# Optimization experiments

Measured on AMD Instinct MI355X. Metric: run time of the kernel, lower is better.

Reference implementation:

```python
import jax, jax.numpy as jnp
import numpy as np

D_MODEL = 1024
NUM_HEADS = 16
HEAD_DIM = D_MODEL // NUM_HEADS
B, S = 2, 2048
EPS = 1e-8


def setup_inputs() -> dict:
    key = jax.random.key(0)
    ks = jax.random.split(key, 9)
    sc = 1.0 / np.sqrt(D_MODEL)
    return {
        "x": jax.random.normal(ks[0], (B, S, D_MODEL), jnp.float32),
        "wq": jax.random.normal(ks[1], (D_MODEL, D_MODEL), jnp.float32) * sc,
        "bq": jax.random.normal(ks[2], (D_MODEL,), jnp.float32) * 0.01,
        "wk": jax.random.normal(ks[3], (D_MODEL, D_MODEL), jnp.float32) * sc,
        "bk": jax.random.normal(ks[4], (D_MODEL,), jnp.float32) * 0.01,
        "wv": jax.random.normal(ks[5], (D_MODEL, D_MODEL), jnp.float32) * sc,
        "bv": jax.random.normal(ks[6], (D_MODEL,), jnp.float32) * 0.01,
        "wo": jax.random.normal(ks[7], (D_MODEL, D_MODEL), jnp.float32) * sc,
        "bo": jax.random.normal(ks[8], (D_MODEL,), jnp.float32) * 0.01,
    }


def reference(x, wq, bq, wk, bk, wv, bv, wo, bo):
    b, s, d = x.shape
    h, hd = NUM_HEADS, HEAD_DIM
    # projections (torch Linear: y = x W^T + b); reshape to [b, h, s, hd]
    def proj(w, bias):
        return (jnp.einsum('bsd,ed->bse', x, w) + bias).reshape(b, s, h, hd).transpose(0, 2, 1, 3)
    q = proj(wq, bq)
    k = proj(wk, bk)
    v = proj(wv, bv)
    scores = jnp.einsum('bhqd,bhkd->bhqk', q, k) / np.sqrt(hd)
    attn = jax.nn.softmax(scores, axis=-1)
    o = jnp.einsum('bhqk,bhkd->bhqd', attn, v)  # [b, h, s, hd]
    # per-position, per-head Gram-Schmidt exclusion: remove component of o[i]
    # along v[i] (the loop in the original is independent over positions)
    v_norm_sq = jnp.sum(v * v, axis=-1, keepdims=True)          # [b,h,s,1]
    align = jnp.sum(o * v, axis=-1, keepdims=True) / (v_norm_sq + EPS)
    o = o - align * v
    o = o.transpose(0, 2, 1, 3).reshape(b, s, d)
    return jnp.einsum('bsd,ed->bse', o, wo) + bo
```

## Files before the change

### kernel.cpp

```cpp
#include <hip/hip_runtime.h>
#include <stdint.h>

#define SEQ 2048
#define NTOK 4096
#define DM 1024

typedef __bf16 bf16x8 __attribute__((ext_vector_type(8)));
typedef __bf16 bf16x4 __attribute__((ext_vector_type(4)));
typedef float f32x4 __attribute__((ext_vector_type(4)));

__device__ __forceinline__ unsigned short f2bf(float f) {
  union { float f; unsigned u; } v; v.f = f;
  return (unsigned short)((v.u + 0x7fffu + ((v.u >> 16) & 1u)) >> 16);
}
__device__ __forceinline__ float bf2f(unsigned short s) {
  union { unsigned u; float f; } v; v.u = ((unsigned)s) << 16; return v.f;
}
__device__ __forceinline__ unsigned pkbf(float a, float b) {
  union { float f; unsigned u; } x, y; x.f = a; y.f = b;
  return __builtin_amdgcn_perm(y.u + 0x8000u, x.u + 0x8000u, 0x07060302u);
}

__device__ __forceinline__ void async16(const unsigned short* g, unsigned short* l) {
  __builtin_amdgcn_global_load_lds(
      (const __attribute__((address_space(1))) void*)g,
      (__attribute__((address_space(3))) void*)l, 16, 0, 0);
}

__global__ __launch_bounds__(256) void cast_all(
    const float* __restrict__ x, const float* __restrict__ wq,
    const float* __restrict__ wk, const float* __restrict__ wv,
    const float* __restrict__ wo, unsigned short* __restrict__ dst) {
  size_t i = ((size_t)blockIdx.x * 256 + threadIdx.x) * 4;
  const float* src; size_t off;
  if (i < (size_t)NTOK * DM) { src = x; off = i; }
  else {
    size_t j = i - (size_t)NTOK * DM;
    int s = (int)(j >> 20);
    src = (s == 0) ? wq : (s == 1) ? wk : (s == 2) ? wv : wo;
    off = j & 1048575u;
  }
  float4 f = *(const float4*)(src + off);
  ushort4 o;
  o.x = f2bf(f.x); o.y = f2bf(f.y); o.z = f2bf(f.z); o.w = f2bf(f.w);
  *(ushort4*)(dst + i) = o;
}

__device__ __forceinline__ void gemm128_core(
    const unsigned short* __restrict__ A, const unsigned short* __restrict__ Bw,
    int m0, int n0, f32x4 acc[4][4], unsigned short* As, unsigned short* Bs) {
  const int tid = threadIdx.x;
  const int lane = tid & 63;
  const int w = tid >> 6;
  const int wm = (w >> 1) * 64, wn = (w & 1) * 64;
  const int quad = lane >> 4, l16 = lane & 15;
  const int srow = tid >> 2, scol = (tid & 3) * 8;

  for (int kt = 0; kt < 1024; kt += 32) {
    __syncthreads();
    async16(A + (size_t)(m0 + srow) * 1024 + kt + scol, As + srow * 32 + scol);
    async16(A + (size_t)(m0 + 64 + srow) * 1024 + kt + scol, As + (64 + srow) * 32 + scol);
    async16(Bw + (size_t)(n0 + srow) * 1024 + kt + scol, Bs + srow * 32 + scol);
    async16(Bw + (size_t)(n0 + 64 + srow) * 1024 + kt + scol, Bs + (64 + srow) * 32 + scol);
    __syncthreads();
    bf16x8 af[4], bf[4];
#pragma unroll
    for (int i = 0; i < 4; ++i)
      af[i] = *(const bf16x8*)(As + (wm + i * 16 + l16) * 32 + quad * 8);
#pragma unroll
    for (int j = 0; j < 4; ++j)
      bf[j] = *(const bf16x8*)(Bs + (wn + j * 16 + l16) * 32 + quad * 8);
#pragma unroll
    for (int i = 0; i < 4; ++i)
#pragma unroll
      for (int j = 0; j < 4; ++j)
        acc[i][j] = __builtin_amdgcn_mfma_f32_16x16x32_bf16(af[i], bf[j], acc[i][j], 0, 0, 0);
  }
}

__global__ __launch_bounds__(256) void qkv_gemm(
    const unsigned short* __restrict__ xb,
    const unsigned short* __restrict__ wqb, const unsigned short* __restrict__ wkb,
    const unsigned short* __restrict__ wvb,
    const float* __restrict__ bq, const float* __restrict__ bk, const float* __restrict__ bv,
    unsigned short* __restrict__ Q, unsigned short* __restrict__ Kd,
    unsigned short* __restrict__ Vt) {
  __shared__ unsigned short As[128 * 32], Bs[128 * 32];
  const int kind = blockIdx.z;
  const unsigned short* A; const unsigned short* Bw;
  int m0, n0;
  if (kind == 2) { A = wvb; Bw = xb; m0 = blockIdx.x * 128; n0 = blockIdx.y * 128; }
  else { A = xb; Bw = (kind == 0) ? wqb : wkb; m0 = blockIdx.y * 128; n0 = blockIdx.x * 128; }
  f32x4 acc[4][4];
#pragma unroll
  for (int i = 0; i < 4; ++i)
#pragma unroll
    for (int j = 0; j < 4; ++j) { f32x4 z = {0.f, 0.f, 0.f, 0.f}; acc[i][j] = z; }
  gemm128_core(A, Bw, m0, n0, acc, As, Bs);

  const int lane = threadIdx.x & 63, w = threadIdx.x >> 6;
  const int quad = lane >> 4, l16 = lane & 15;
  const int wm = (w >> 1) * 64, wn = (w & 1) * 64;

  if (kind == 2) {
#pragma unroll
    for (int i = 0; i < 4; ++i)
#pragma unroll
      for (int j = 0; j < 4; ++j) {
        const int n = n0 + wn + j * 16 + l16;
        const int tb = n >> 11, s = n & 2047;
#pragma unroll
        for (int r = 0; r < 4; ++r) {
          const int m = m0 + wm + i * 16 + quad * 4 + r;
          const int h = m >> 6, d = m & 63;
          Vt[((size_t)(tb * 16 + h) * 64 + d) * SEQ + s] = f2bf(acc[i][j][r] + bv[m]);
        }
      }
  } else {
    const float* bias = (kind == 0) ? bq : bk;
    const float scale = (kind == 0) ? 0.180336880f : 1.0f;
#pragma unroll
    for (int i = 0; i < 4; ++i)
#pragma unroll
      for (int j = 0; j < 4; ++j) {
        const int col = n0 + wn + j * 16 + l16;
        const float bb = bias[col];
        const int h = col >> 6, d = col & 63;
#pragma unroll
        for (int r = 0; r < 4; ++r) {
          const int m = m0 + wm + i * 16 + quad * 4 + r;
          const int b = m >> 11, s = m & 2047;
          const int bh = b * 16 + h;
          const unsigned short val = f2bf((acc[i][j][r] + bb) * scale);
          if (kind == 0) Q[((size_t)bh * SEQ + s) * 64 + d] = val;
          else           Kd[((size_t)bh * SEQ + s) * 64 + d] = val;
        }
      }
  }
}

__global__ __launch_bounds__(256) void attn_kernel(
    const unsigned short* __restrict__ Q, const unsigned short* __restrict__ Kd,
    const unsigned short* __restrict__ Vt,
    unsigned short* __restrict__ Op, float* __restrict__ Lp) {
  __shared__ unsigned short KV[4][4096];
  const int gx = blockIdx.x;
  const int xcd = gx & 7;
  const int idx = gx >> 3;
  const int bh  = xcd * 4 + (idx & 3);
  const int ksl = (idx >> 2) & 1;
  const int q0  = ((idx >> 3) & 15) * 128;
  const int ks0 = ksl << 10;
  const int tid = threadIdx.x, lane = tid & 63, w = tid >> 6;
  const int quad = lane >> 4, l16 = lane & 15;
  const unsigned short* Qp = Q + (size_t)bh * SEQ * 64;
  const unsigned short* Kp = Kd + (size_t)bh * SEQ * 64;
  const unsigned short* Vp = Vt + (size_t)bh * 64 * SEQ;
  const int srow = tid >> 3;
  const int sc = ((tid & 7) ^ (srow & 7)) << 3;

#pragma unroll
  for (int c = 0; c < 4; ++c)
    async16(Qp + (size_t)(q0 + c * 32 + srow) * 64 + sc,
            KV[(c < 2) ? 1 : 3] + (c & 1) * 2048 + tid * 8);
  async16(Kp + (size_t)(ks0 + srow) * 64 + sc, KV[0] + tid * 8);
  async16(Kp + (size_t)(ks0 + 32 + srow) * 64 + sc, KV[0] + 2048 + tid * 8);
  async16(Vp + (size_t)srow * SEQ + ks0 + sc, KV[2] + tid * 8);
  async16(Vp + (size_t)(32 + srow) * SEQ + ks0 + sc, KV[2] + 2048 + tid * 8);
  __syncthreads();

  const int sel = l16 & 7;
  const unsigned short* Qsrc = (w < 2) ? KV[1] : KV[3];
  bf16x8 bQ[2][2];
#pragma unroll
  for (int qq = 0; qq < 2; ++qq) {
    const int qrow = (w * 32 + qq * 16 + l16) & 63;
#pragma unroll
    for (int hh = 0; hh < 2; ++hh)
      bQ[qq][hh] = *(const bf16x8*)(Qsrc + qrow * 64 + (((hh * 4 + quad) ^ sel) << 3));
  }
  __syncthreads();

  union { unsigned short u[8]; bf16x8 v; } one8;
#pragma unroll
  for (int t = 0; t < 8; ++t) one8.u[t] = 0x3F80;
  const bf16x8 aOnes = one8.v;

  f32x4 o_acc[2][4];
  f32x4 l_acc[2];
  const f32x4 zinit = {-12.f, -12.f, -12.f, -12.f};
#pragma unroll
  for (int qq = 0; qq < 2; ++qq) {
    f32x4 z = {0.f, 0.f, 0.f, 0.f};
    l_acc[qq] = z;
#pragma unroll
    for (int dt = 0; dt < 4; ++dt) o_acc[qq][dt] = z;
  }

  for (int it = 0; it < 16; ++it) {
    const int cur = it & 1;
    if (it) __syncthreads();
    if (it + 1 < 16) {
      const int kt = ks0 + (it + 1) * 64, nb = (it + 1) & 1;
      async16(Kp + (size_t)(kt + srow) * 64 + sc, KV[nb] + tid * 8);
      async16(Kp + (size_t)(kt + 32 + srow) * 64 + sc, KV[nb] + 2048 + tid * 8);
      async16(Vp + (size_t)srow * SEQ + kt + sc, KV[2 + nb] + tid * 8);
      async16(Vp + (size_t)(32 + srow) * SEQ + kt + sc, KV[2 + nb] + 2048 + tid * 8);
    }
    const unsigned short* Ks = KV[cur];
    const unsigned short* Vs = KV[2 + cur];

    f32x4 st[2][4];
#pragma unroll
    for (int kk = 0; kk < 4; ++kk) {
      const int krow = kk * 16 + l16;
      bf16x8 a0 = *(const bf16x8*)(Ks + krow * 64 + ((quad ^ sel) << 3));
      bf16x8 a1 = *(const bf16x8*)(Ks + krow * 64 + (((4 + quad) ^ sel) << 3));
#pragma unroll
      for (int qq = 0; qq < 2; ++qq) {
        f32x4 z = __builtin_amdgcn_mfma_f32_16x16x32_bf16(a0, bQ[qq][0], zinit, 0, 0, 0);
        z = __builtin_amdgcn_mfma_f32_16x16x32_bf16(a1, bQ[qq][1], z, 0, 0, 0);
        st[qq][kk] = z;
      }
    }

    bf16x8 bP[2][2];
#pragma unroll
    for (int qq = 0; qq < 2; ++qq) {
#pragma unroll
      for (int kk = 0; kk < 4; ++kk)
#pragma unroll
        for (int r = 0; r < 4; ++r)
          st[qq][kk][r] = __builtin_amdgcn_exp2f(st[qq][kk][r]);
#pragma unroll
      for (int G = 0; G < 2; ++G) {
        union { unsigned d[4]; bf16x8 v; } pk;
        pk.d[0] = pkbf(st[qq][2 * G][0], st[qq][2 * G][1]);
        pk.d[1] = pkbf(st[qq][2 * G][2], st[qq][2 * G][3]);
        pk.d[2] = pkbf(st[qq][2 * G + 1][0], st[qq][2 * G + 1][1]);
        pk.d[3] = pkbf(st[qq][2 * G + 1][2], st[qq][2 * G + 1][3]);
        bP[qq][G] = pk.v;
      }
    }

#pragma unroll
    for (int qq = 0; qq < 2; ++qq)
#pragma unroll
      for (int G = 0; G < 2; ++G)
        l_acc[qq] = __builtin_amdgcn_mfma_f32_16x16x32_bf16(aOnes, bP[qq][G], l_acc[qq], 0, 0, 0);

#pragma unroll
    for (int dt = 0; dt < 4; ++dt) {
      const unsigned short* vbase = Vs + (dt * 16 + l16) * 64;
      const int inner = (quad & 1) * 4;
#pragma unroll
      for (int G = 0; G < 2; ++G) {
        const int c0 = 4 * G + (quad >> 1);
        bf16x4 lo = *(const bf16x4*)(vbase + ((c0 ^ sel) << 3) + inner);
        bf16x4 hi = *(const bf16x4*)(vbase + (((c0 + 2) ^ sel) << 3) + inner);
        bf16x8 aV = __builtin_shufflevector(lo, hi, 0, 1, 2, 3, 4, 5, 6, 7);
#pragma unroll
        for (int qq = 0; qq < 2; ++qq)
          o_acc[qq][dt] = __builtin_amdgcn_mfma_f32_16x16x32_bf16(aV, bP[qq][G], o_acc[qq][dt], 0, 0, 0);
      }
    }
  }

  const size_t sb = (size_t)(ksl * 32 + bh);
#pragma unroll
  for (int qq = 0; qq < 2; ++qq) {
    const int qg = q0 + w * 32 + qq * 16 + l16;
#pragma unroll
    for (int dt = 0; dt < 4; ++dt)
#pragma unroll
      for (int r = 0; r < 4; ++r) {
        const int d = dt * 16 + quad * 4 + r;
        Op[(sb * 64 + d) * SEQ + qg] = f2bf(o_acc[qq][dt][r]);
      }
    if (quad == 0) Lp[sb * SEQ + qg] = l_acc[qq][0];
  }
}

__global__ __launch_bounds__(128) void combine_kernel(
    const unsigned short* __restrict__ Op, const float* __restrict__ Lp,
    const unsigned short* __restrict__ Vt, unsigned short* __restrict__ O) {
  const int bh = blockIdx.y;
  const int q = blockIdx.x * 128 + threadIdx.x;
  const size_t QC = (size_t)32 * SEQ;
  const size_t idx = (size_t)bh * SEQ + q;
  const float inv = 1.0f / (Lp[idx] + Lp[QC + idx]);
  const unsigned short* O1 = Op + (size_t)bh * 64 * SEQ + q;
  const unsigned short* O2 = O1 + QC * 64;
  const unsigned short* Vp = Vt + (size_t)bh * 64 * SEQ + q;
  float o64[64];
  float ov = 0.f, vv = 0.f;
#pragma unroll
  for (int d = 0; d < 64; ++d) {
    const float o = (bf2f(O1[(size_t)d * SEQ]) + bf2f(O2[(size_t)d * SEQ])) * inv;
    const float v = bf2f(Vp[(size_t)d * SEQ]);
    o64[d] = o; ov += o * v; vv += v * v;
  }
  const float align = ov / (vv + 1e-8f);
  const int b = bh >> 4, h = bh & 15;
  unsigned short* dst = O + (size_t)(b * SEQ + q) * DM + h * 64;
#pragma unroll
  for (int d = 0; d < 64; d += 2) {
    const float a0 = o64[d]     - align * bf2f(Vp[(size_t)d * SEQ]);
    const float a1 = o64[d + 1] - align * bf2f(Vp[(size_t)(d + 1) * SEQ]);
    *(unsigned*)(dst + d) = pkbf(a0, a1);
  }
}

__global__ __launch_bounds__(256) void out_gemm(
    const unsigned short* __restrict__ Ob, const unsigned short* __restrict__ wob,
    const float* __restrict__ bo, float* __restrict__ out) {
  __shared__ unsigned short As[64 * 32], Bs[128 * 32];
  const int m0 = blockIdx.y * 64, n0 = blockIdx.x * 128;
  const int tid = threadIdx.x, lane = tid & 63, w = tid >> 6;
  const int wm = (w >> 1) * 32, wn = (w & 1) * 64;
  const int quad = lane >> 4, l16 = lane & 15;
  const int srow = tid >> 2, scol = (tid & 3) * 8;
  f32x4 acc[2][4];
#pragma unroll
  for (int i = 0; i < 2; ++i)
#pragma unroll
    for (int j = 0; j < 4; ++j) { f32x4 z = {0.f, 0.f, 0.f, 0.f}; acc[i][j] = z; }

  for (int kt = 0; kt < 1024; kt += 32) {
    __syncthreads();
    async16(Ob + (size_t)(m0 + srow) * 1024 + kt + scol, As + srow * 32 + scol);
    async16(wob + (size_t)(n0 + srow) * 1024 + kt + scol, Bs + srow * 32 + scol);
    async16(wob + (size_t)(n0 + 64 + srow) * 1024 + kt + scol, Bs + (64 + srow) * 32 + scol);
    __syncthreads();
    bf16x8 af[2], bf[4];
#pragma unroll
    for (int i = 0; i < 2; ++i)
      af[i] = *(const bf16x8*)(As + (wm + i * 16 + l16) * 32 + quad * 8);
#pragma unroll
    for (int j = 0; j < 4; ++j)
      bf[j] = *(const bf16x8*)(Bs + (wn + j * 16 + l16) * 32 + quad * 8);
#pragma unroll
    for (int i = 0; i < 2; ++i)
#pragma unroll
      for (int j = 0; j < 4; ++j)
        acc[i][j] = __builtin_amdgcn_mfma_f32_16x16x32_bf16(af[i], bf[j], acc[i][j], 0, 0, 0);
  }

#pragma unroll
  for (int i = 0; i < 2; ++i)
#pragma unroll
    for (int j = 0; j < 4; ++j) {
      const int col = n0 + wn + j * 16 + l16;
      const float bb = bo[col];
#pragma unroll
      for (int r = 0; r < 4; ++r) {
        const int m = m0 + wm + i * 16 + quad * 4 + r;
        out[(size_t)m * DM + col] = acc[i][j][r] + bb;
      }
    }
}

extern "C" void kernel_launch(void* const* d_in, const int* in_sizes, int n_in,
                              void* d_out, int out_size, void* d_ws, size_t ws_size,
                              hipStream_t stream) {
  const float* x  = (const float*)d_in[0];
  const float* wq = (const float*)d_in[1];
  const float* bq = (const float*)d_in[2];
  const float* wk = (const float*)d_in[3];
  const float* bk = (const float*)d_in[4];
  const float* wv = (const float*)d_in[5];
  const float* bv = (const float*)d_in[6];
  const float* wo = (const float*)d_in[7];
  const float* bo = (const float*)d_in[8];
  float* out = (float*)d_out;
  (void)in_sizes; (void)n_in; (void)out_size; (void)ws_size;

  unsigned short* ws  = (unsigned short*)d_ws;
  unsigned short* xb  = ws;
  unsigned short* wqb = xb + (size_t)NTOK * DM;
  unsigned short* wkb = wqb + (size_t)DM * DM;
  unsigned short* wvb = wkb + (size_t)DM * DM;
  unsigned short* wob = wvb + (size_t)DM * DM;
  unsigned short* Qb  = wob + (size_t)DM * DM;
  unsigned short* Kb  = Qb + (size_t)NTOK * DM;
  unsigned short* Vtb = Kb + (size_t)NTOK * DM;
  unsigned short* Ob  = Vtb + (size_t)NTOK * DM;
  unsigned short* Opb = Ob + (size_t)NTOK * DM;
  float* Lpw = (float*)(Opb + (size_t)2 * 32 * 64 * SEQ);

  cast_all<<<8192, 256, 0, stream>>>(x, wq, wk, wv, wo, ws);
  qkv_gemm<<<dim3(8, 32, 3), 256, 0, stream>>>(xb, wqb, wkb, wvb, bq, bk, bv, Qb, Kb, Vtb);
  attn_kernel<<<1024, 256, 0, stream>>>(Qb, Kb, Vtb, Opb, Lpw);
  combine_kernel<<<dim3(16, 32), 128, 0, stream>>>(Opb, Lpw, Vtb, Ob);
  out_gemm<<<dim3(8, 64), 256, 0, stream>>>(Ob, wob, bo, out);
}
```

Before: 211.2 us.

## Double GEMM K-tile to 64 with swizzled LDS and widen attention query tile

The QKV and output GEMMs now stage 64-wide K slices, using an XOR-swizzled LDS layout. This halves the number of barrier-separated iterations and is meant to avoid bank conflicts on fragment reads. The attention kernel now gives each block 256 queries, with 64 per wave, launches half as many blocks, and fuses the exp/pack step into the score loop. This amortizes K/V tile loads over more queries, at the cost of more registers (launch bounds 256,2) and fewer blocks for load balancing.

```diff
diff --git a/kernel.cpp b/kernel.cpp
--- a/kernel.cpp
+++ b/kernel.cpp
@@ -46,35 +46,39 @@
   *(ushort4*)(dst + i) = o;
 }
 
-__device__ __forceinline__ void gemm128_core(
+__device__ __forceinline__ void gemm128_bk64(
     const unsigned short* __restrict__ A, const unsigned short* __restrict__ Bw,
     int m0, int n0, f32x4 acc[4][4], unsigned short* As, unsigned short* Bs) {
-  const int tid = threadIdx.x;
-  const int lane = tid & 63;
-  const int w = tid >> 6;
+  const int tid = threadIdx.x, lane = tid & 63, w = tid >> 6;
   const int wm = (w >> 1) * 64, wn = (w & 1) * 64;
-  const int quad = lane >> 4, l16 = lane & 15;
-  const int srow = tid >> 2, scol = (tid & 3) * 8;
-
-  for (int kt = 0; kt < 1024; kt += 32) {
+  const int quad = lane >> 4, l16 = lane & 15, sel = l16 & 7;
+  const int srow = tid >> 3;
+  const int sc = ((tid & 7) ^ (srow & 7)) << 3;
+
+  for (int kt = 0; kt < 1024; kt += 64) {
     __syncthreads();
-    async16(A + (size_t)(m0 + srow) * 1024 + kt + scol, As + srow * 32 + scol);
-    async16(A + (size_t)(m0 + 64 + srow) * 1024 + kt + scol, As + (64 + srow) * 32 + scol);
-    async16(Bw + (size_t)(n0 + srow) * 1024 + kt + scol, Bs + srow * 32 + scol);
-    async16(Bw + (size_t)(n0 + 64 + srow) * 1024 + kt + scol, Bs + (64 + srow) * 32 + scol);
+#pragma unroll
+    for (int c = 0; c < 4; ++c) {
+      const int row = c * 32 + srow;
+      async16(A + (size_t)(m0 + row) * 1024 + kt + sc, As + c * 2048 + tid * 8);
+      async16(Bw + (size_t)(n0 + row) * 1024 + kt + sc, Bs + c * 2048 + tid * 8);
+    }
     __syncthreads();
-    bf16x8 af[4], bf[4];
-#pragma unroll
-    for (int i = 0; i < 4; ++i)
-      af[i] = *(const bf16x8*)(As + (wm + i * 16 + l16) * 32 + quad * 8);
-#pragma unroll
-    for (int j = 0; j < 4; ++j)
-      bf[j] = *(const bf16x8*)(Bs + (wn + j * 16 + l16) * 32 + quad * 8);
-#pragma unroll
-    for (int i = 0; i < 4; ++i)
+#pragma unroll
+    for (int ks = 0; ks < 2; ++ks) {
+      bf16x8 af[4], bf[4];
+#pragma unroll
+      for (int i = 0; i < 4; ++i)
+        af[i] = *(const bf16x8*)(As + (wm + i * 16 + l16) * 64 + (((ks * 4 + quad) ^ sel) << 3));
 #pragma unroll
       for (int j = 0; j < 4; ++j)
-        acc[i][j] = __builtin_amdgcn_mfma_f32_16x16x32_bf16(af[i], bf[j], acc[i][j], 0, 0, 0);
+        bf[j] = *(const bf16x8*)(Bs + (wn + j * 16 + l16) * 64 + (((ks * 4 + quad) ^ sel) << 3));
+#pragma unroll
+      for (int i = 0; i < 4; ++i)
+#pragma unroll
+        for (int j = 0; j < 4; ++j)
+          acc[i][j] = __builtin_amdgcn_mfma_f32_16x16x32_bf16(af[i], bf[j], acc[i][j], 0, 0, 0);
+    }
   }
 }
 
@@ -85,7 +89,7 @@
     const float* __restrict__ bq, const float* __restrict__ bk, const float* __restrict__ bv,
     unsigned short* __restrict__ Q, unsigned short* __restrict__ Kd,
     unsigned short* __restrict__ Vt) {
-  __shared__ unsigned short As[128 * 32], Bs[128 * 32];
+  __shared__ unsigned short As[128 * 64], Bs[128 * 64];
   const int kind = blockIdx.z;
   const unsigned short* A; const unsigned short* Bw;
   int m0, n0;
@@ -96,7 +100,7 @@
   for (int i = 0; i < 4; ++i)
 #pragma unroll
     for (int j = 0; j < 4; ++j) { f32x4 z = {0.f, 0.f, 0.f, 0.f}; acc[i][j] = z; }
-  gemm128_core(A, Bw, m0, n0, acc, As, Bs);
+  gemm128_bk64(A, Bw, m0, n0, acc, As, Bs);
 
   const int lane = threadIdx.x & 63, w = threadIdx.x >> 6;
   const int quad = lane >> 4, l16 = lane & 15;
@@ -139,7 +143,7 @@
   }
 }
 
-__global__ __launch_bounds__(256) void attn_kernel(
+__global__ __launch_bounds__(256, 2) void attn_kernel(
     const unsigned short* __restrict__ Q, const unsigned short* __restrict__ Kd,
     const unsigned short* __restrict__ Vt,
     unsigned short* __restrict__ Op, float* __restrict__ Lp) {
@@ -149,7 +153,7 @@
   const int idx = gx >> 3;
   const int bh  = xcd * 4 + (idx & 3);
   const int ksl = (idx >> 2) & 1;
-  const int q0  = ((idx >> 3) & 15) * 128;
+  const int q0  = (idx >> 3) * 256;
   const int ks0 = ksl << 10;
   const int tid = threadIdx.x, lane = tid & 63, w = tid >> 6;
   const int quad = lane >> 4, l16 = lane & 15;
@@ -160,37 +164,38 @@
   const int sc = ((tid & 7) ^ (srow & 7)) << 3;
 
 #pragma unroll
-  for (int c = 0; c < 4; ++c)
+  for (int c = 0; c < 8; ++c)
     async16(Qp + (size_t)(q0 + c * 32 + srow) * 64 + sc,
-            KV[(c < 2) ? 1 : 3] + (c & 1) * 2048 + tid * 8);
+            KV[c >> 1] + (c & 1) * 2048 + tid * 8);
+  __syncthreads();
+
+  const int sel = l16 & 7;
+  const unsigned short* Qsrc = KV[w];
+  bf16x8 bQ[4][2];
+#pragma unroll
+  for (int qq = 0; qq < 4; ++qq) {
+    const int qrow = qq * 16 + l16;
+#pragma unroll
+    for (int hh = 0; hh < 2; ++hh)
+      bQ[qq][hh] = *(const bf16x8*)(Qsrc + qrow * 64 + (((hh * 4 + quad) ^ sel) << 3));
+  }
+  __syncthreads();
+
   async16(Kp + (size_t)(ks0 + srow) * 64 + sc, KV[0] + tid * 8);
   async16(Kp + (size_t)(ks0 + 32 + srow) * 64 + sc, KV[0] + 2048 + tid * 8);
   async16(Vp + (size_t)srow * SEQ + ks0 + sc, KV[2] + tid * 8);
   async16(Vp + (size_t)(32 + srow) * SEQ + ks0 + sc, KV[2] + 2048 + tid * 8);
-  __syncthreads();
-
-  const int sel = l16 & 7;
-  const unsigned short* Qsrc = (w < 2) ? KV[1] : KV[3];
-  bf16x8 bQ[2][2];
-#pragma unroll
-  for (int qq = 0; qq < 2; ++qq) {
-    const int qrow = (w * 32 + qq * 16 + l16) & 63;
-#pragma unroll
-    for (int hh = 0; hh < 2; ++hh)
-      bQ[qq][hh] = *(const bf16x8*)(Qsrc + qrow * 64 + (((hh * 4 + quad) ^ sel) << 3));
-  }
-  __syncthreads();
 
   union { unsigned short u[8]; bf16x8 v; } one8;
 #pragma unroll
   for (int t = 0; t < 8; ++t) one8.u[t] = 0x3F80;
   const bf16x8 aOnes = one8.v;
 
-  f32x4 o_acc[2][4];
-  f32x4 l_acc[2];
+  f32x4 o_acc[4][4];
+  f32x4 l_acc[4];
   const f32x4 zinit = {-12.f, -12.f, -12.f, -12.f};
 #pragma unroll
-  for (int qq = 0; qq < 2; ++qq) {
+  for (int qq = 0; qq < 4; ++qq) {
     f32x4 z = {0.f, 0.f, 0.f, 0.f};
     l_acc[qq] = z;
 #pragma unroll
@@ -199,7 +204,7 @@
 
   for (int it = 0; it < 16; ++it) {
     const int cur = it & 1;
-    if (it) __syncthreads();
+    __syncthreads();
     if (it + 1 < 16) {
       const int kt = ks0 + (it + 1) * 64, nb = (it + 1) & 1;
       async16(Kp + (size_t)(kt + srow) * 64 + sc, KV[nb] + tid * 8);
@@ -210,41 +215,30 @@
     const unsigned short* Ks = KV[cur];
     const unsigned short* Vs = KV[2 + cur];
 
-    f32x4 st[2][4];
+    bf16x8 bP[4][2];
 #pragma unroll
     for (int kk = 0; kk < 4; ++kk) {
       const int krow = kk * 16 + l16;
       bf16x8 a0 = *(const bf16x8*)(Ks + krow * 64 + ((quad ^ sel) << 3));
       bf16x8 a1 = *(const bf16x8*)(Ks + krow * 64 + (((4 + quad) ^ sel) << 3));
 #pragma unroll
-      for (int qq = 0; qq < 2; ++qq) {
+      for (int qq = 0; qq < 4; ++qq) {
         f32x4 z = __builtin_amdgcn_mfma_f32_16x16x32_bf16(a0, bQ[qq][0], zinit, 0, 0, 0);
         z = __builtin_amdgcn_mfma_f32_16x16x32_bf16(a1, bQ[qq][1], z, 0, 0, 0);
-        st[qq][kk] = z;
-      }
-    }
-
-    bf16x8 bP[2][2];
-#pragma unroll
-    for (int qq = 0; qq < 2; ++qq) {
-#pragma unroll
-      for (int kk = 0; kk < 4; ++kk)
-#pragma unroll
-        for (int r = 0; r < 4; ++r)
-          st[qq][kk][r] = __builtin_amdgcn_exp2f(st[qq][kk][r]);
-#pragma unroll
-      for (int G = 0; G < 2; ++G) {
+#pragma unroll
+        for (int r = 0; r < 4; ++r) z[r] = __builtin_amdgcn_exp2f(z[r]);
+        unsigned lo = pkbf(z[0], z[1]);
+        unsigned hi = pkbf(z[2], z[3]);
         union { unsigned d[4]; bf16x8 v; } pk;
-        pk.d[0] = pkbf(st[qq][2 * G][0], st[qq][2 * G][1]);
-        pk.d[1] = pkbf(st[qq][2 * G][2], st[qq][2 * G][3]);
-        pk.d[2] = pkbf(st[qq][2 * G + 1][0], st[qq][2 * G + 1][1]);
-        pk.d[3] = pkbf(st[qq][2 * G + 1][2], st[qq][2 * G + 1][3]);
-        bP[qq][G] = pk.v;
-      }
-    }
-
-#pragma unroll
-    for (int qq = 0; qq < 2; ++qq)
+        pk.v = bP[qq][kk >> 1];
+        pk.d[(kk & 1) * 2] = lo;
+        pk.d[(kk & 1) * 2 + 1] = hi;
+        bP[qq][kk >> 1] = pk.v;
+      }
+    }
+
+#pragma unroll
+    for (int qq = 0; qq < 4; ++qq)
 #pragma unroll
       for (int G = 0; G < 2; ++G)
         l_acc[qq] = __builtin_amdgcn_mfma_f32_16x16x32_bf16(aOnes, bP[qq][G], l_acc[qq], 0, 0, 0);
@@ -260,7 +254,7 @@
         bf16x4 hi = *(const bf16x4*)(vbase + (((c0 + 2) ^ sel) << 3) + inner);
         bf16x8 aV = __builtin_shufflevector(lo, hi, 0, 1, 2, 3, 4, 5, 6, 7);
 #pragma unroll
-        for (int qq = 0; qq < 2; ++qq)
+        for (int qq = 0; qq < 4; ++qq)
           o_acc[qq][dt] = __builtin_amdgcn_mfma_f32_16x16x32_bf16(aV, bP[qq][G], o_acc[qq][dt], 0, 0, 0);
       }
     }
@@ -268,8 +262,8 @@
 
   const size_t sb = (size_t)(ksl * 32 + bh);
 #pragma unroll
-  for (int qq = 0; qq < 2; ++qq) {
-    const int qg = q0 + w * 32 + qq * 16 + l16;
+  for (int qq = 0; qq < 4; ++qq) {
+    const int qg = q0 + w * 64 + qq * 16 + l16;
 #pragma unroll
     for (int dt = 0; dt < 4; ++dt)
 #pragma unroll
@@ -314,36 +308,47 @@
 __global__ __launch_bounds__(256) void out_gemm(
     const unsigned short* __restrict__ Ob, const unsigned short* __restrict__ wob,
     const float* __restrict__ bo, float* __restrict__ out) {
-  __shared__ unsigned short As[64 * 32], Bs[128 * 32];
+  __shared__ unsigned short As[64 * 64], Bs[128 * 64];
   const int m0 = blockIdx.y * 64, n0 = blockIdx.x * 128;
   const int tid = threadIdx.x, lane = tid & 63, w = tid >> 6;
   const int wm = (w >> 1) * 32, wn = (w & 1) * 64;
-  const int quad = lane >> 4, l16 = lane & 15;
-  const int srow = tid >> 2, scol = (tid & 3) * 8;
+  const int quad = lane >> 4, l16 = lane & 15, sel = l16 & 7;
+  const int srow = tid >> 3;
+  const int sc = ((tid & 7) ^ (srow & 7)) << 3;
   f32x4 acc[2][4];
 #pragma unroll
   for (int i = 0; i < 2; ++i)
 #pragma unroll
     for (int j = 0; j < 4; ++j) { f32x4 z = {0.f, 0.f, 0.f, 0.f}; acc[i][j] = z; }
 
-  for (int kt = 0; kt < 1024; kt += 32) {
+  for (int kt = 0; kt < 1024; kt += 64) {
     __syncthreads();
-    async16(Ob + (size_t)(m0 + srow) * 1024 + kt + scol, As + srow * 32 + scol);
-    async16(wob + (size_t)(n0 + srow) * 1024 + kt + scol, Bs + srow * 32 + scol);
-    async16(wob + (size_t)(n0 + 64 + srow) * 1024 + kt + scol, Bs + (64 + srow) * 32 + scol);
+#pragma unroll
+    for (int c = 0; c < 2; ++c) {
+      const int row = c * 32 + srow;
+      async16(Ob + (size_t)(m0 + row) * 1024 + kt + sc, As + c * 2048 + tid * 8);
+    }
+#pragma unroll
+    for (int c = 0; c < 4; ++c) {
+      const int row = c * 32 + srow;
+      async16(wob + (size_t)(n0 + row) * 1024 + kt + sc, Bs + c * 2048 + tid * 8);
+    }
     __syncthreads();
-    bf16x8 af[2], bf[4];
-#pragma unroll
-    for (int i = 0; i < 2; ++i)
-      af[i] = *(const bf16x8*)(As + (wm + i * 16 + l16) * 32 + quad * 8);
-#pragma unroll
-    for (int j = 0; j < 4; ++j)
-      bf[j] = *(const bf16x8*)(Bs + (wn + j * 16 + l16) * 32 + quad * 8);
-#pragma unroll
-    for (int i = 0; i < 2; ++i)
+#pragma unroll
+    for (int ks = 0; ks < 2; ++ks) {
+      bf16x8 af[2], bf[4];
+#pragma unroll
+      for (int i = 0; i < 2; ++i)
+        af[i] = *(const bf16x8*)(As + (wm + i * 16 + l16) * 64 + (((ks * 4 + quad) ^ sel) << 3));
 #pragma unroll
       for (int j = 0; j < 4; ++j)
-        acc[i][j] = __builtin_amdgcn_mfma_f32_16x16x32_bf16(af[i], bf[j], acc[i][j], 0, 0, 0);
+        bf[j] = *(const bf16x8*)(Bs + (wn + j * 16 + l16) * 64 + (((ks * 4 + quad) ^ sel) << 3));
+#pragma unroll
+      for (int i = 0; i < 2; ++i)
+#pragma unroll
+        for (int j = 0; j < 4; ++j)
+          acc[i][j] = __builtin_amdgcn_mfma_f32_16x16x32_bf16(af[i], bf[j], acc[i][j], 0, 0, 0);
+    }
   }
 
 #pragma unroll
@@ -390,7 +395,7 @@
 
   cast_all<<<8192, 256, 0, stream>>>(x, wq, wk, wv, wo, ws);
   qkv_gemm<<<dim3(8, 32, 3), 256, 0, stream>>>(xb, wqb, wkb, wvb, bq, bk, bv, Qb, Kb, Vtb);
-  attn_kernel<<<1024, 256, 0, stream>>>(Qb, Kb, Vtb, Opb, Lpw);
+  attn_kernel<<<512, 256, 0, stream>>>(Qb, Kb, Vtb, Opb, Lpw);
   combine_kernel<<<dim3(16, 32), 128, 0, stream>>>(Opb, Lpw, Vtb, Ob);
   out_gemm<<<dim3(8, 64), 256, 0, stream>>>(Ob, wob, bo, out);
 }
```

After: 197.1 us. -6.7%, faster.
